# Performance work log

Measured on AMD Instinct MI355X. Metric: run time of the kernel, lower is better.

## Reference

```python
import jax, jax.numpy as jnp
import numpy as np

N_HEADS = 12
N_GROUPS = 32
EPS = 1e-5


def setup_inputs() -> dict:
    key = jax.random.key(0)
    ks = jax.random.split(key, 6)
    B, C, H, W = 8, 768, 32, 32
    EC, S = 768, 256
    x = jax.random.normal(ks[0], (B, C, H, W), dtype=jnp.float32)
    encoder_out = jax.random.normal(ks[1], (B, EC, S), dtype=jnp.float32)
    gn_w = jnp.ones((C,), jnp.float32)
    gn_b = jnp.zeros((C,), jnp.float32)
    qkv_w = jax.random.normal(ks[2], (3 * C, C), dtype=jnp.float32) * 0.02
    qkv_b = jnp.zeros((3 * C,), jnp.float32)
    enc_w = jax.random.normal(ks[3], (2 * C, EC), dtype=jnp.float32) * 0.02
    enc_b = jnp.zeros((2 * C,), jnp.float32)
    proj_w = jax.random.normal(ks[4], (C, C), dtype=jnp.float32) * 0.02
    proj_b = jnp.zeros((C,), jnp.float32)
    return {"x": x, "encoder_out": encoder_out, "gn_w": gn_w, "gn_b": gn_b,
            "qkv_w": qkv_w, "qkv_b": qkv_b, "enc_w": enc_w, "enc_b": enc_b,
            "proj_w": proj_w, "proj_b": proj_b}


def _group_norm(x, w, b):
    # x: [B, C, T]
    B, C, T = x.shape
    xg = x.reshape(B, N_GROUPS, C // N_GROUPS, T)
    mean = jnp.mean(xg, axis=(2, 3), keepdims=True)
    var = jnp.var(xg, axis=(2, 3), keepdims=True)
    xn = ((xg - mean) * jax.lax.rsqrt(var + EPS)).reshape(B, C, T)
    return xn * w[None, :, None] + b[None, :, None]


def reference(x, encoder_out, gn_w, gn_b, qkv_w, qkv_b, enc_w, enc_b, proj_w, proj_b):
    B, C, Hs, Ws = x.shape
    T = Hs * Ws
    ch = C // N_HEADS
    xf = x.reshape(B, C, T)
    xn = _group_norm(xf, gn_w, gn_b)
    # 1x1 conv == channel matmul
    qkv = jnp.einsum('oc,bct->bot', qkv_w, xn) + qkv_b[None, :, None]  # [B, 3C, T]
    # torch layout: per-head contiguous blocks of [q, k, v]
    qkv = qkv.reshape(B * N_HEADS, 3 * ch, T)
    q, k, v = qkv[:, :ch], qkv[:, ch:2 * ch], qkv[:, 2 * ch:]
    ekv = jnp.einsum('oc,bcs->bos', enc_w, encoder_out) + enc_b[None, :, None]  # [B, 2C, S]
    ekv = ekv.reshape(B * N_HEADS, 2 * ch, -1)
    ek, ev = ekv[:, :ch], ekv[:, ch:]
    k = jnp.concatenate([ek, k], axis=-1)  # [BH, ch, S+T]
    v = jnp.concatenate([ev, v], axis=-1)
    scale = 1.0 / np.sqrt(np.sqrt(ch))
    w = jnp.einsum('bct,bcs->bts', q * scale, k * scale)  # [BH, T, S+T]
    w = jax.nn.softmax(w.astype(jnp.float32), axis=-1).astype(q.dtype)
    a = jnp.einsum('bts,bcs->bct', w, v).reshape(B, C, T)
    h = jnp.einsum('oc,bct->bot', proj_w, a) + proj_b[None, :, None]
    return (xf + h).reshape(B, C, Hs, Ws)
```

## Files before the change

kernel.cpp:

```cpp
#include <hip/hip_runtime.h>

typedef __attribute__((ext_vector_type(8))) short bf16x8;
typedef __attribute__((ext_vector_type(4))) float f32x4;
typedef __attribute__((ext_vector_type(16))) float f32x16;
typedef __attribute__((ext_vector_type(4))) float float4v;
typedef __attribute__((ext_vector_type(4))) unsigned short ushort4v;
typedef __attribute__((ext_vector_type(8))) unsigned short ushort8v;

#define DEVINL __device__ __forceinline__


DEVINL unsigned short f2bf(float f) {
  union { float f; unsigned u; } v; v.f = f;
  unsigned r = (v.u + 0x7fffu + ((v.u >> 16) & 1u)) >> 16;
  return (unsigned short)r;
}
DEVINL float bf2f(unsigned short h) {
  union { unsigned u; float f; } v; v.u = ((unsigned)h) << 16;
  return v.f;
}
DEVINL float exp2a(float x) {
  float r; asm("v_exp_f32 %0, %1" : "=v"(r) : "v"(x)); return r;
}
DEVINL unsigned cvtpk(float lo, float hi) {
  unsigned r;
  asm("v_cvt_pk_bf16_f32 %0, %1, %2" : "=v"(r) : "v"(lo), "v"(hi));
  return r;
}
DEVINL void gload16(const void* g, void* l) {
  __builtin_amdgcn_global_load_lds(
      (const __attribute__((address_space(1))) unsigned*)g,
      (__attribute__((address_space(3))) unsigned*)l, 16, 0, 0);
}
DEVINL void plswap(unsigned& a, unsigned& b) {
  asm("v_permlane32_swap_b32 %0, %1" : "+v"(a), "+v"(b));
}
DEVINL bf16x8 mkfrag(unsigned a, unsigned b, unsigned c, unsigned d) {
  union { unsigned u[4]; bf16x8 v; } x;
  x.u[0] = a; x.u[1] = b; x.u[2] = c; x.u[3] = d;
  return x.v;
}

__global__ __launch_bounds__(256) void k_cvt3(const float* __restrict__ s0,
                                              const float* __restrict__ s1,
                                              const float* __restrict__ s2,
                                              unsigned short* __restrict__ d) {
  int i = blockIdx.x * 256 + threadIdx.x;
  const float* s; int off;
  if (i < 442368)      { s = s0; off = i; }
  else if (i < 737280) { s = s1; off = i - 442368; }
  else                 { s = s2; off = i - 737280; }
  float4v v = *(const float4v*)(s + (size_t)off * 4);
  ushort4v o;
  o[0] = f2bf(v[0]); o[1] = f2bf(v[1]); o[2] = f2bf(v[2]); o[3] = f2bf(v[3]);
  *(ushort4v*)(d + (size_t)i * 4) = o;
}

__global__ __launch_bounds__(256) void k_gn(const float* __restrict__ x,
                                            const float* __restrict__ gw,
                                            const float* __restrict__ gb,
                                            unsigned short* __restrict__ xnt) {
  int g = blockIdx.x, b = blockIdx.y, tid = threadIdx.x;
  const float* xb = x + ((size_t)b * 768 + g * 24) * 1024;
  float s = 0.f, ss = 0.f;
  for (int i = tid; i < 6144; i += 256) {
    float4v v = *(const float4v*)(xb + (size_t)i * 4);
    s += v[0] + v[1] + v[2] + v[3];
    ss += v[0] * v[0] + v[1] * v[1] + v[2] * v[2] + v[3] * v[3];
  }
  #pragma unroll
  for (int o = 32; o > 0; o >>= 1) { s += __shfl_down(s, o); ss += __shfl_down(ss, o); }
  __shared__ float rs[4], rss[4], stat[2];
  int w = tid >> 6;
  if ((tid & 63) == 0) { rs[w] = s; rss[w] = ss; }
  __syncthreads();
  if (tid == 0) {
    float S = rs[0] + rs[1] + rs[2] + rs[3], SS = rss[0] + rss[1] + rss[2] + rss[3];
    float mean = S / 24576.f;
    float var = SS / 24576.f - mean * mean;
    stat[0] = mean; stat[1] = rsqrtf(fmaxf(var, 0.f) + 1e-5f);
  }
  __syncthreads();
  float mean = stat[0], rstd = stat[1];
  float wv[24], bv[24];
  #pragma unroll
  for (int c = 0; c < 24; ++c) { wv[c] = gw[g * 24 + c]; bv[c] = gb[g * 24 + c]; }
  for (int it = 0; it < 4; ++it) {
    int t = it * 256 + tid;
    ushort8v ov[3];
    #pragma unroll
    for (int c = 0; c < 24; ++c) {
      float v = xb[(size_t)c * 1024 + t];
      ov[c >> 3][c & 7] = f2bf((v - mean) * rstd * wv[c] + bv[c]);
    }
    ushort8v* dst = (ushort8v*)(xnt + ((size_t)(b * 1024 + t)) * 768 + g * 24);
    dst[0] = ov[0]; dst[1] = ov[1]; dst[2] = ov[2];
  }
}

__global__ __launch_bounds__(256) void k_enc_tr(const float* __restrict__ enc,
                                                unsigned short* __restrict__ et) {
  int ct = blockIdx.x * 64, st = blockIdx.y * 64, b = blockIdx.z, tid = threadIdx.x;
  __shared__ unsigned short L[64 * 72];
  #pragma unroll
  for (int it = 0; it < 4; ++it) {
    int idx = it * 256 + tid; int r = idx >> 4, ch = idx & 15;
    float4v v = *(const float4v*)(enc + ((size_t)(b * 768 + ct + r)) * 256 + st + ch * 4);
    ushort4v o;
    o[0] = f2bf(v[0]); o[1] = f2bf(v[1]); o[2] = f2bf(v[2]); o[3] = f2bf(v[3]);
    *(ushort4v*)&L[r * 72 + ch * 4] = o;
  }
  __syncthreads();
  #pragma unroll
  for (int it = 0; it < 2; ++it) {
    int idx = it * 256 + tid; int s = idx >> 3, ch = idx & 7;
    ushort8v o;
    #pragma unroll
    for (int j = 0; j < 8; ++j) o[j] = L[(ch * 8 + j) * 72 + s];
    *(ushort8v*)(et + ((size_t)(b * 256 + st + s)) * 768 + ct + ch * 8) = o;
  }
}

__global__ __launch_bounds__(256) void k_vcat(const unsigned short* __restrict__ qkvt,
                                              const unsigned short* __restrict__ ekvt,
                                              unsigned short* __restrict__ vcat) {
  int s0 = blockIdx.x * 64, bh = blockIdx.y, b = bh / 12, h = bh % 12, tid = threadIdx.x;
  __shared__ unsigned short L[64 * 72];
  #pragma unroll
  for (int it = 0; it < 2; ++it) {
    int idx = it * 256 + tid; int s = idx >> 3, ch = idx & 7;
    int sg = s0 + s;
    const unsigned short* src = (sg < 256)
        ? ekvt + ((size_t)(b * 256 + sg)) * 1536 + h * 128 + 64 + ch * 8
        : qkvt + ((size_t)(b * 1024 + sg - 256)) * 2304 + h * 192 + 128 + ch * 8;
    *(ushort8v*)&L[s * 72 + ch * 8] = *(const ushort8v*)src;
  }
  __syncthreads();
  #pragma unroll
  for (int it = 0; it < 2; ++it) {
    int idx = it * 256 + tid; int c = idx >> 3, ch = idx & 7;
    ushort8v o;
    #pragma unroll
    for (int j = 0; j < 8; ++j) o[j] = L[(ch * 8 + j) * 72 + c];
    *(ushort8v*)(vcat + ((size_t)bh * 64 + c) * 1280 + s0 + ch * 8) = o;
  }
}

template <int EPI>
__global__ __launch_bounds__(256, 2) void k_gemm(const unsigned short* __restrict__ A,
                                                 const unsigned short* __restrict__ B,
                                                 const float* __restrict__ bias,
                                                 const float* __restrict__ resid,
                                                 void* __restrict__ outp,
                                                 int N, int K,
                                                 long sA, long sB, long sO, long sR) {
  int bz = blockIdx.z;
  int m0 = blockIdx.x * 128, n0 = blockIdx.y * 128;
  const unsigned short* Ab = A + (size_t)bz * sA + (size_t)m0 * K;
  const unsigned short* Bb = B + (size_t)bz * sB + (size_t)n0 * K;
  __shared__ unsigned short As[2][8192], Bs[2][8192];
  int tid = threadIdx.x, lane = tid & 63, w = tid >> 6;
  int ln = lane & 15, lg = lane >> 4;
  int wm = (w >> 1) * 64, wn = (w & 1) * 64;
  int srow = tid >> 3;
  int schunk = ((tid & 7) ^ (srow & 7)) * 8;
  const unsigned short* gA = Ab + (size_t)srow * K + schunk;
  const unsigned short* gB = Bb + (size_t)srow * K + schunk;

  f32x4 acc[4][4];
  #pragma unroll
  for (int i = 0; i < 4; ++i)
    #pragma unroll
    for (int j = 0; j < 4; ++j) acc[i][j] = (f32x4){0.f, 0.f, 0.f, 0.f};

  auto stageAB = [&](int buf, int k0) {
    #pragma unroll
    for (int it = 0; it < 4; ++it)
      gload16(gA + (size_t)it * 32 * K + k0, &As[buf][it * 2048 + w * 512]);
    #pragma unroll
    for (int it = 0; it < 4; ++it)
      gload16(gB + (size_t)it * 32 * K + k0, &Bs[buf][it * 2048 + w * 512]);
  };

  stageAB(0, 0);
  asm volatile("s_waitcnt vmcnt(0)" ::: "memory");
  __syncthreads();

  int nk = K >> 6;
  for (int kt = 0; kt < nk; ++kt) {
    int cur = kt & 1;
    if (kt + 1 < nk) stageAB(cur ^ 1, (kt + 1) * 64);
    #pragma unroll
    for (int kk = 0; kk < 2; ++kk) {
      bf16x8 af[4], bfv[4];
      #pragma unroll
      for (int i = 0; i < 4; ++i)
        af[i] = *(const bf16x8*)&As[cur][(wm + i * 16 + ln) * 64 + (((kk * 4 + lg) ^ (ln & 7)) * 8)];
      #pragma unroll
      for (int j = 0; j < 4; ++j)
        bfv[j] = *(const bf16x8*)&Bs[cur][(wn + j * 16 + ln) * 64 + (((kk * 4 + lg) ^ (ln & 7)) * 8)];
      __builtin_amdgcn_s_setprio(1);
      #pragma unroll
      for (int i = 0; i < 4; ++i)
        #pragma unroll
        for (int j = 0; j < 4; ++j)
          acc[i][j] = __builtin_amdgcn_mfma_f32_16x16x32_bf16(af[i], bfv[j], acc[i][j], 0, 0, 0);
      __builtin_amdgcn_s_setprio(0);
    }
    if (kt + 1 < nk) asm volatile("s_waitcnt vmcnt(0)" ::: "memory");
    __syncthreads();
  }

  #pragma unroll
  for (int i = 0; i < 4; ++i) {
    #pragma unroll
    for (int j = 0; j < 4; ++j) {
      #pragma unroll
      for (int r = 0; r < 4; ++r) {
        int row = m0 + wm + i * 16 + lg * 4 + r;
        int col = n0 + wn + j * 16 + ln;
        float v = acc[i][j][r];
        if (EPI == 0) {
          v += bias[col];
          ((unsigned short*)outp)[(size_t)bz * sO + (size_t)row * N + col] = f2bf(v);
        } else {
          v += bias[row] + resid[(size_t)bz * sR + (size_t)row * N + col];
          ((float*)outp)[(size_t)bz * sO + (size_t)row * N + col] = v;
        }
      }
    }
  }
}

__global__ __launch_bounds__(256, 3) void k_attn(const unsigned short* __restrict__ qkvt,
                                                 const unsigned short* __restrict__ ekvt,
                                                 const unsigned short* __restrict__ vcat,
                                                 unsigned short* __restrict__ at) {
  int bid = blockIdx.x;
  int swb = (bid & 7) * 96 + (bid >> 3);
  int t0 = (swb & 7) * 128, bh = swb >> 3, b = bh / 12, h = bh % 12;
  int tid = threadIdx.x, w = tid >> 6, lane = tid & 63;
  int ql = lane & 31, hi = lane >> 5;
  __shared__ unsigned short Ks[2][4096], Vs[2][4096];

  const float QSC = 0.125f * 1.44269504089f;
  bf16x8 aq[4];
  const unsigned short* qrow = qkvt + ((size_t)(b * 1024 + t0 + w * 32 + ql)) * 2304 + h * 192;
  #pragma unroll
  for (int jc = 0; jc < 4; ++jc) {
    ushort8v qv = *(const ushort8v*)(qrow + jc * 16 + hi * 8);
    bf16x8 o;
    #pragma unroll
    for (int e = 0; e < 8; ++e) o[e] = (short)f2bf(bf2f(qv[e]) * QSC);
    aq[jc] = o;
  }

  int rloc = w * 16 + (lane >> 3);
  int chunk = (lane & 7) ^ (lane >> 3);
  const unsigned short* ke_st = ekvt + ((size_t)(b * 256 + rloc)) * 1536 + h * 128 + chunk * 8;
  const unsigned short* kq_st = qkvt + ((long)b * 1024 - 256 + rloc) * 2304 + h * 192 + 64 + chunk * 8;
  const unsigned short* v_st  = vcat + ((size_t)(bh * 64 + rloc)) * 1280 + chunk * 8;
  unsigned short* kd = &Ks[0][0] + w * 1024;
  unsigned short* vd = &Vs[0][0] + w * 1024;

  auto stage = [&](int nb, int tn) {
    const unsigned short* ks;
    size_t rstep;
    if (tn < 4) { ks = ke_st + (size_t)tn * 64 * 1536; rstep = 8 * 1536; }
    else        { ks = kq_st + (size_t)tn * 64 * 2304; rstep = 8 * 2304; }
    unsigned short* kdd = kd + nb * 4096;
    unsigned short* vdd = vd + nb * 4096;
    const unsigned short* vs = v_st + tn * 64;
    gload16(ks, kdd);
    gload16(ks + rstep, kdd + 512);
    gload16(vs, vdd);
    gload16(vs + 8 * 1280, vdd + 512);
  };

  stage(0, 0);
  asm volatile("s_waitcnt vmcnt(0)" ::: "memory");
  __syncthreads();

  f32x16 acc0, acc1;
  #pragma unroll
  for (int r = 0; r < 16; ++r) { acc0[r] = 0.f; acc1[r] = 0.f; }
  float m = 0.f, l = 0.f;
  int xp = (ql & 7) << 4;

  for (int t = 0; t < 20; ++t) {
    int cur = t & 1;
    if (t < 19) stage(cur ^ 1, t + 1);

    f32x16 sf0, sf1;
    #pragma unroll
    for (int r = 0; r < 16; ++r) { sf0[r] = 0.f; sf1[r] = 0.f; }
    const char* kbase = (const char*)&Ks[cur][0] + ql * 128;
    __builtin_amdgcn_s_setprio(1);
    #pragma unroll
    for (int jc = 0; jc < 4; ++jc) {
      int off = (jc * 32 + hi * 16) ^ xp;
      bf16x8 k0f = *(const bf16x8*)(kbase + off);
      bf16x8 k1f = *(const bf16x8*)(kbase + 4096 + off);
      sf0 = __builtin_amdgcn_mfma_f32_32x32x16_bf16(k0f, aq[jc], sf0, 0, 0, 0);
      sf1 = __builtin_amdgcn_mfma_f32_32x32x16_bf16(k1f, aq[jc], sf1, 0, 0, 0);
    }
    __builtin_amdgcn_s_setprio(0);

    float pe[32];
    #pragma unroll
    for (int i = 0; i < 16; ++i) pe[i] = exp2a(sf0[i] - m);
    #pragma unroll
    for (int i = 0; i < 16; ++i) pe[16 + i] = exp2a(sf1[i] - m);

    const char* vbase = (const char*)&Vs[cur][0] + ql * 128;
    #pragma unroll
    for (int sb = 0; sb < 2; ++sb) {
      unsigned pk[8];
      #pragma unroll
      for (int i = 0; i < 8; ++i)
        pk[i] = cvtpk(pe[sb * 16 + 2 * i], pe[sb * 16 + 2 * i + 1]);
      plswap(pk[0], pk[2]);
      plswap(pk[1], pk[3]);
      plswap(pk[4], pk[6]);
      plswap(pk[5], pk[7]);
      bf16x8 fj0 = mkfrag(pk[0], pk[1], pk[2], pk[3]);
      bf16x8 fj1 = mkfrag(pk[4], pk[5], pk[6], pk[7]);
      __builtin_amdgcn_s_setprio(1);
      #pragma unroll
      for (int jj = 0; jj < 2; ++jj) {
        int off = (sb * 64 + jj * 32 + hi * 16) ^ xp;
        bf16x8 v0f = *(const bf16x8*)(vbase + off);
        bf16x8 v1f = *(const bf16x8*)(vbase + 4096 + off);
        bf16x8 pf = jj ? fj1 : fj0;
        acc0 = __builtin_amdgcn_mfma_f32_32x32x16_bf16(v0f, pf, acc0, 0, 0, 0);
        acc1 = __builtin_amdgcn_mfma_f32_32x32x16_bf16(v1f, pf, acc1, 0, 0, 0);
      }
      __builtin_amdgcn_s_setprio(0);
    }

    float s0 = 0.f, s1 = 0.f, s2 = 0.f, s3 = 0.f;
    #pragma unroll
    for (int i = 0; i < 8; ++i) {
      s0 += pe[i]; s1 += pe[8 + i]; s2 += pe[16 + i]; s3 += pe[24 + i];
    }
    l += (s0 + s1) + (s2 + s3);

    float mx[8];
    #pragma unroll
    for (int i = 0; i < 8; ++i)
      mx[i] = fmaxf(fmaxf(pe[i], pe[i + 8]), fmaxf(pe[i + 16], pe[i + 24]));
    #pragma unroll
    for (int o = 4; o > 0; o >>= 1)
      #pragma unroll
      for (int i = 0; i < 4; ++i)
        if (i < o) mx[i] = fmaxf(mx[i], mx[i + o]);
    float pmax = fmaxf(mx[0], __shfl_xor(mx[0], 32));
    if (!__all(pmax <= 256.f)) {
      float mn = m + __log2f(fmaxf(pmax, 1.f));
      float al = exp2a(m - mn);
      l *= al;
      #pragma unroll
      for (int r = 0; r < 16; ++r) { acc0[r] *= al; acc1[r] *= al; }
      m = mn;
    }

    if (t < 19) asm volatile("s_waitcnt vmcnt(0)" ::: "memory");
    __syncthreads();
  }

  l += __shfl_xor(l, 32);
  float rl = 1.f / l;
  unsigned short* orow = at + ((size_t)(b * 1024 + t0 + w * 32 + ql)) * 768 + h * 64;
  #pragma unroll
  for (int cb = 0; cb < 2; ++cb) {
    #pragma unroll
    for (int g = 0; g < 4; ++g) {
      int c = cb * 32 + g * 8 + hi * 4;
      ushort4v o;
      #pragma unroll
      for (int i = 0; i < 4; ++i) {
        float v = (cb ? acc1[g * 4 + i] : acc0[g * 4 + i]) * rl;
        o[i] = f2bf(v);
      }
      *(ushort4v*)(orow + c) = o;
    }
  }
}

extern "C" void kernel_launch(void* const* d_in, const int* in_sizes, int n_in,
                              void* d_out, int out_size, void* d_ws, size_t ws_size,
                              hipStream_t stream) {
  const float* x      = (const float*)d_in[0];
  const float* enc    = (const float*)d_in[1];
  const float* gn_w   = (const float*)d_in[2];
  const float* gn_b   = (const float*)d_in[3];
  const float* qkv_w  = (const float*)d_in[4];
  const float* qkv_b  = (const float*)d_in[5];
  const float* enc_w  = (const float*)d_in[6];
  const float* enc_b  = (const float*)d_in[7];
  const float* proj_w = (const float*)d_in[8];
  const float* proj_b = (const float*)d_in[9];
  float* out = (float*)d_out;

  char* ws = (char*)d_ws;
  unsigned short* w_qkv = (unsigned short*)(ws + 0);
  unsigned short* w_enc = (unsigned short*)(ws + 3538944);
  unsigned short* w_prj = (unsigned short*)(ws + 5898240);
  unsigned short* xn_t  = (unsigned short*)(ws + 7077888);
  unsigned short* enc_t = (unsigned short*)(ws + 19660800);
  unsigned short* qkv_t = (unsigned short*)(ws + 22806528);
  unsigned short* ekv_t = (unsigned short*)(ws + 60555264);
  unsigned short* vcat  = (unsigned short*)(ws + 66846720);
  unsigned short* a_t   = xn_t;

  k_cvt3<<<3456, 256, 0, stream>>>(qkv_w, enc_w, proj_w, w_qkv);
  k_gn<<<dim3(32, 8), 256, 0, stream>>>(x, gn_w, gn_b, xn_t);
  k_enc_tr<<<dim3(12, 4, 8), 256, 0, stream>>>(enc, enc_t);
  k_gemm<0><<<dim3(64, 18, 1), 256, 0, stream>>>(xn_t, w_qkv, qkv_b, nullptr, qkv_t,
                                                 2304, 768, 0L, 0L, 0L, 0L);
  k_gemm<0><<<dim3(16, 12, 1), 256, 0, stream>>>(enc_t, w_enc, enc_b, nullptr, ekv_t,
                                                 1536, 768, 0L, 0L, 0L, 0L);
  k_vcat<<<dim3(20, 96), 256, 0, stream>>>(qkv_t, ekv_t, vcat);
  k_attn<<<dim3(768), 256, 0, stream>>>(qkv_t, ekv_t, vcat, a_t);
  k_gemm<1><<<dim3(6, 8, 8), 256, 0, stream>>>(w_prj, a_t, proj_b, x, out,
                                               1024, 768, 0L, 786432L, 786432L, 786432L);
}
```

Measured before the change: 173.4 us.

## Triple-buffer LDS staging in GEMM and attention with one barrier per step

Both the GEMM and attention kernels move from double-buffered to triple-buffered LDS, keeping two tiles in flight. Each step waits only for the oldest tile (vmcnt(4)) and then hits a single raw barrier, instead of draining every load before the barrier. The GEMM K-tile shrinks from 64 to 32 with a 4-wide XOR swizzle, and its occupancy hint goes from 2 to 3 blocks, keeping LDS use about the same. The cost is more loop iterations and barriers in the GEMM, and more LDS per attention block, which may lower attention occupancy.

```diff
diff --git a/kernel.cpp b/kernel.cpp
--- a/kernel.cpp
+++ b/kernel.cpp
@@ -40,6 +40,9 @@
   x.u[0] = a; x.u[1] = b; x.u[2] = c; x.u[3] = d;
   return x.v;
 }
+#define WAITV4 asm volatile("s_waitcnt vmcnt(4)" ::: "memory")
+#define WAITV0 asm volatile("s_waitcnt vmcnt(0)" ::: "memory")
+#define RBAR  do { __builtin_amdgcn_s_barrier(); __builtin_amdgcn_sched_barrier(0); } while (0)
 
 __global__ __launch_bounds__(256) void k_cvt3(const float* __restrict__ s0,
                                               const float* __restrict__ s1,
@@ -147,7 +150,7 @@
 }
 
 template <int EPI>
-__global__ __launch_bounds__(256, 2) void k_gemm(const unsigned short* __restrict__ A,
+__global__ __launch_bounds__(256, 3) void k_gemm(const unsigned short* __restrict__ A,
                                                  const unsigned short* __restrict__ B,
                                                  const float* __restrict__ bias,
                                                  const float* __restrict__ resid,
@@ -158,14 +161,14 @@
   int m0 = blockIdx.x * 128, n0 = blockIdx.y * 128;
   const unsigned short* Ab = A + (size_t)bz * sA + (size_t)m0 * K;
   const unsigned short* Bb = B + (size_t)bz * sB + (size_t)n0 * K;
-  __shared__ unsigned short As[2][8192], Bs[2][8192];
+  __shared__ unsigned short As[3][4096], Bs[3][4096];
   int tid = threadIdx.x, lane = tid & 63, w = tid >> 6;
   int ln = lane & 15, lg = lane >> 4;
   int wm = (w >> 1) * 64, wn = (w & 1) * 64;
-  int srow = tid >> 3;
-  int schunk = ((tid & 7) ^ (srow & 7)) * 8;
-  const unsigned short* gA = Ab + (size_t)srow * K + schunk;
-  const unsigned short* gB = Bb + (size_t)srow * K + schunk;
+  int sr = tid >> 2, sc = tid & 3;
+  const unsigned short* gA = Ab + (size_t)sr * K + ((sc ^ (sr & 3)) * 8);
+  const unsigned short* gB = Bb + (size_t)sr * K + ((sc ^ (sr & 3)) * 8);
+  int swz = (lg ^ (ln & 3)) * 8;
 
   f32x4 acc[4][4];
   #pragma unroll
@@ -174,42 +177,47 @@
     for (int j = 0; j < 4; ++j) acc[i][j] = (f32x4){0.f, 0.f, 0.f, 0.f};
 
   auto stageAB = [&](int buf, int k0) {
-    #pragma unroll
-    for (int it = 0; it < 4; ++it)
-      gload16(gA + (size_t)it * 32 * K + k0, &As[buf][it * 2048 + w * 512]);
-    #pragma unroll
-    for (int it = 0; it < 4; ++it)
-      gload16(gB + (size_t)it * 32 * K + k0, &Bs[buf][it * 2048 + w * 512]);
+    unsigned short* ad = &As[buf][0] + w * 512;
+    unsigned short* bd = &Bs[buf][0] + w * 512;
+    gload16(gA + k0, ad);
+    gload16(gA + (size_t)64 * K + k0, ad + 2048);
+    gload16(gB + k0, bd);
+    gload16(gB + (size_t)64 * K + k0, bd + 2048);
   };
-
+  auto comp = [&](int buf) {
+    bf16x8 af[4], bfv[4];
+    #pragma unroll
+    for (int i = 0; i < 4; ++i) af[i] = *(const bf16x8*)&As[buf][(wm + i * 16 + ln) * 32 + swz];
+    #pragma unroll
+    for (int j = 0; j < 4; ++j) bfv[j] = *(const bf16x8*)&Bs[buf][(wn + j * 16 + ln) * 32 + swz];
+    __builtin_amdgcn_s_setprio(1);
+    #pragma unroll
+    for (int i = 0; i < 4; ++i)
+      #pragma unroll
+      for (int j = 0; j < 4; ++j)
+        acc[i][j] = __builtin_amdgcn_mfma_f32_16x16x32_bf16(af[i], bfv[j], acc[i][j], 0, 0, 0);
+    __builtin_amdgcn_s_setprio(0);
+  };
+
+  int nk = K >> 5;
   stageAB(0, 0);
-  asm volatile("s_waitcnt vmcnt(0)" ::: "memory");
-  __syncthreads();
-
-  int nk = K >> 6;
-  for (int kt = 0; kt < nk; ++kt) {
-    int cur = kt & 1;
-    if (kt + 1 < nk) stageAB(cur ^ 1, (kt + 1) * 64);
-    #pragma unroll
-    for (int kk = 0; kk < 2; ++kk) {
-      bf16x8 af[4], bfv[4];
-      #pragma unroll
-      for (int i = 0; i < 4; ++i)
-        af[i] = *(const bf16x8*)&As[cur][(wm + i * 16 + ln) * 64 + (((kk * 4 + lg) ^ (ln & 7)) * 8)];
-      #pragma unroll
-      for (int j = 0; j < 4; ++j)
-        bfv[j] = *(const bf16x8*)&Bs[cur][(wn + j * 16 + ln) * 64 + (((kk * 4 + lg) ^ (ln & 7)) * 8)];
-      __builtin_amdgcn_s_setprio(1);
-      #pragma unroll
-      for (int i = 0; i < 4; ++i)
-        #pragma unroll
-        for (int j = 0; j < 4; ++j)
-          acc[i][j] = __builtin_amdgcn_mfma_f32_16x16x32_bf16(af[i], bfv[j], acc[i][j], 0, 0, 0);
-      __builtin_amdgcn_s_setprio(0);
-    }
-    if (kt + 1 < nk) asm volatile("s_waitcnt vmcnt(0)" ::: "memory");
-    __syncthreads();
-  }
+  stageAB(1, 32);
+  WAITV4;
+  RBAR;
+  int cur = 0;
+  for (int kt = 0; kt < nk - 2; ++kt) {
+    int pre = cur - 1; if (pre < 0) pre += 3;
+    stageAB(pre, (kt + 2) * 32);
+    comp(cur);
+    WAITV4;
+    RBAR;
+    ++cur; if (cur == 3) cur = 0;
+  }
+  comp(cur);
+  WAITV0;
+  RBAR;
+  ++cur; if (cur == 3) cur = 0;
+  comp(cur);
 
   #pragma unroll
   for (int i = 0; i < 4; ++i) {
@@ -241,7 +249,7 @@
   int t0 = (swb & 7) * 128, bh = swb >> 3, b = bh / 12, h = bh % 12;
   int tid = threadIdx.x, w = tid >> 6, lane = tid & 63;
   int ql = lane & 31, hi = lane >> 5;
-  __shared__ unsigned short Ks[2][4096], Vs[2][4096];
+  __shared__ unsigned short Ks[3][4096], Vs[3][4096];
 
   const float QSC = 0.125f * 1.44269504089f;
   bf16x8 aq[4];
@@ -260,16 +268,14 @@
   const unsigned short* ke_st = ekvt + ((size_t)(b * 256 + rloc)) * 1536 + h * 128 + chunk * 8;
   const unsigned short* kq_st = qkvt + ((long)b * 1024 - 256 + rloc) * 2304 + h * 192 + 64 + chunk * 8;
   const unsigned short* v_st  = vcat + ((size_t)(bh * 64 + rloc)) * 1280 + chunk * 8;
-  unsigned short* kd = &Ks[0][0] + w * 1024;
-  unsigned short* vd = &Vs[0][0] + w * 1024;
 
   auto stage = [&](int nb, int tn) {
     const unsigned short* ks;
     size_t rstep;
     if (tn < 4) { ks = ke_st + (size_t)tn * 64 * 1536; rstep = 8 * 1536; }
     else        { ks = kq_st + (size_t)tn * 64 * 2304; rstep = 8 * 2304; }
-    unsigned short* kdd = kd + nb * 4096;
-    unsigned short* vdd = vd + nb * 4096;
+    unsigned short* kdd = &Ks[nb][0] + w * 1024;
+    unsigned short* vdd = &Vs[nb][0] + w * 1024;
     const unsigned short* vs = v_st + tn * 64;
     gload16(ks, kdd);
     gload16(ks + rstep, kdd + 512);
@@ -277,24 +283,17 @@
     gload16(vs + 8 * 1280, vdd + 512);
   };
 
-  stage(0, 0);
-  asm volatile("s_waitcnt vmcnt(0)" ::: "memory");
-  __syncthreads();
-
   f32x16 acc0, acc1;
   #pragma unroll
   for (int r = 0; r < 16; ++r) { acc0[r] = 0.f; acc1[r] = 0.f; }
   float m = 0.f, l = 0.f;
   int xp = (ql & 7) << 4;
 
-  for (int t = 0; t < 20; ++t) {
-    int cur = t & 1;
-    if (t < 19) stage(cur ^ 1, t + 1);
-
+  auto comp = [&](int buf) {
     f32x16 sf0, sf1;
     #pragma unroll
     for (int r = 0; r < 16; ++r) { sf0[r] = 0.f; sf1[r] = 0.f; }
-    const char* kbase = (const char*)&Ks[cur][0] + ql * 128;
+    const char* kbase = (const char*)&Ks[buf][0] + ql * 128;
     __builtin_amdgcn_s_setprio(1);
     #pragma unroll
     for (int jc = 0; jc < 4; ++jc) {
@@ -312,7 +311,7 @@
     #pragma unroll
     for (int i = 0; i < 16; ++i) pe[16 + i] = exp2a(sf1[i] - m);
 
-    const char* vbase = (const char*)&Vs[cur][0] + ql * 128;
+    const char* vbase = (const char*)&Vs[buf][0] + ql * 128;
     #pragma unroll
     for (int sb = 0; sb < 2; ++sb) {
       unsigned pk[8];
@@ -363,10 +362,26 @@
       for (int r = 0; r < 16; ++r) { acc0[r] *= al; acc1[r] *= al; }
       m = mn;
     }
-
-    if (t < 19) asm volatile("s_waitcnt vmcnt(0)" ::: "memory");
-    __syncthreads();
-  }
+  };
+
+  stage(0, 0);
+  stage(1, 1);
+  WAITV4;
+  RBAR;
+  int cur = 0;
+  for (int t = 0; t < 18; ++t) {
+    int pre = cur - 1; if (pre < 0) pre += 3;
+    stage(pre, t + 2);
+    comp(cur);
+    WAITV4;
+    RBAR;
+    ++cur; if (cur == 3) cur = 0;
+  }
+  comp(cur);
+  WAITV0;
+  RBAR;
+  ++cur; if (cur == 3) cur = 0;
+  comp(cur);
 
   l += __shfl_xor(l, 32);
   float rl = 1.f / l;
```

After: 174.1 us. No clear change (+0.4%).
